# Performance work log

Measured on AMD Instinct MI355X. Metric: run time of the kernel, lower is better.

## Reference

```python
import jax, jax.numpy as jnp
import numpy as np

N_NODES = 100000
N_EDGES = 600000
D = 128
BN_EPS = 1e-5


def setup_inputs() -> dict:
    key = jax.random.key(0)
    k1, k2, k3 = jax.random.split(key, 3)
    x = jax.random.normal(k1, (N_NODES, D), dtype=jnp.float32)
    edge_index = jax.random.randint(k2, (2, N_EDGES), 0, N_NODES, dtype=jnp.int64)
    # Linear(in=D, out=D): kaiming-uniform-ish init
    W = jax.random.normal(k3, (D, D), dtype=jnp.float32) / np.sqrt(D)
    b = jnp.zeros((D,), dtype=jnp.float32)
    eps_gin = jnp.zeros((), dtype=jnp.float32)  # train_eps=True, init 0
    gamma = jnp.ones((D,), dtype=jnp.float32)
    beta = jnp.zeros((D,), dtype=jnp.float32)
    return {"x": x, "edge_index": edge_index, "W": W, "b": b,
            "eps_gin": eps_gin, "gamma": gamma, "beta": beta}


def reference(x, edge_index, W, b, eps_gin, gamma, beta):
    src, dst = edge_index[0], edge_index[1]
    # GIN aggregation: sum of source features into destination nodes
    agg = jax.ops.segment_sum(x[src], dst, num_segments=N_NODES)  # [N, D]
    h = (1.0 + eps_gin) * x + agg
    # MLP([D, D]) == single Linear (PyG plain_last)
    h = jnp.einsum('nd,df->nf', h, W.T) + b  # torch Linear: h @ W^T + b
    # BatchNorm1d in training mode (batch stats, biased variance)
    mean = jnp.mean(h, axis=0)
    var = jnp.mean((h - mean) ** 2, axis=0)
    h = (h - mean) * jax.lax.rsqrt(var + BN_EPS) * gamma + beta
    h = jax.nn.relu(h)
    # residual
    return h + x
```

## Files before the change

kernel.cpp:

```cpp
#include <hip/hip_runtime.h>
#include <hip/hip_bf16.h>

#define N_NODES 100000
#define N_EDGES 600000
#define D 128
#define BN_EPS 1e-5f
#define CAP 32
#define NAGG_BLOCKS 1024

typedef __bf16 bf16x8 __attribute__((ext_vector_type(8)));
typedef float floatx4 __attribute__((ext_vector_type(4)));
typedef unsigned short ushortx8 __attribute__((ext_vector_type(8)));

__device__ __forceinline__ unsigned short f2bf(float f) {
    union { float f; unsigned u; } v; v.f = f;
    unsigned u = v.u;
    unsigned r = u + 0x7FFFu + ((u >> 16) & 1u);
    return (unsigned short)(r >> 16);
}
__device__ __forceinline__ float bflo(unsigned u) {
    union { unsigned u; float f; } v; v.u = u << 16; return v.f;
}
__device__ __forceinline__ float bfhi(unsigned u) {
    union { unsigned u; float f; } v; v.u = u & 0xFFFF0000u; return v.f;
}

__global__ __launch_bounds__(256) void k_fill(const int* __restrict__ ei,
                                              int* __restrict__ cursor,
                                              int* __restrict__ bucket) {
    int e = blockIdx.x * 256 + threadIdx.x;
    if (e >= N_EDGES) return;
    int src = ei[e];
    int dst = ei[N_EDGES + e];
    int pos = atomicAdd(&cursor[dst], 1);
    if (pos < CAP) bucket[dst * CAP + pos] = src;
}

__global__ __launch_bounds__(256) void k_gemm_y(const float* __restrict__ x,
                                                const float* __restrict__ W,
                                                unsigned short* __restrict__ y) {
    const int lane = threadIdx.x & 63;
    const int wid  = threadIdx.x >> 6;
    const int gw   = blockIdx.x * 4 + wid;
    const int fhalf = gw & 1;
    const int chunk = gw >> 1;
    const int n16  = lane & 15;
    const int quad = lane >> 4;
    const int fbase = fhalf * 64;

    bf16x8 B[4][4];
#pragma unroll
    for (int ft = 0; ft < 4; ++ft) {
#pragma unroll
        for (int ks = 0; ks < 4; ++ks) {
            const float* wp = W + (fbase + ft * 16 + n16) * D + ks * 32 + quad * 8;
            float4 wa = *(const float4*)wp;
            float4 wb = *(const float4*)(wp + 4);
            ushortx8 u;
            u[0] = f2bf(wa.x); u[1] = f2bf(wa.y); u[2] = f2bf(wa.z); u[3] = f2bf(wa.w);
            u[4] = f2bf(wb.x); u[5] = f2bf(wb.y); u[6] = f2bf(wb.z); u[7] = f2bf(wb.w);
            B[ft][ks] = __builtin_bit_cast(bf16x8, u);
        }
    }

    const int rbase = chunk * 16;
    floatx4 acc[4];
#pragma unroll
    for (int ft = 0; ft < 4; ++ft) acc[ft] = (floatx4){0.f, 0.f, 0.f, 0.f};

#pragma unroll
    for (int ks = 0; ks < 4; ++ks) {
        const float* xp = x + (size_t)(rbase + n16) * D + ks * 32 + quad * 8;
        float4 xa = *(const float4*)xp;
        float4 xb4 = *(const float4*)(xp + 4);
        ushortx8 u;
        u[0] = f2bf(xa.x); u[1] = f2bf(xa.y); u[2] = f2bf(xa.z); u[3] = f2bf(xa.w);
        u[4] = f2bf(xb4.x); u[5] = f2bf(xb4.y); u[6] = f2bf(xb4.z); u[7] = f2bf(xb4.w);
        bf16x8 a = __builtin_bit_cast(bf16x8, u);
#pragma unroll
        for (int ft = 0; ft < 4; ++ft)
            acc[ft] = __builtin_amdgcn_mfma_f32_16x16x32_bf16(a, B[ft][ks], acc[ft], 0, 0, 0);
    }

#pragma unroll
    for (int ft = 0; ft < 4; ++ft) {
        const int col = fbase + ft * 16 + n16;
#pragma unroll
        for (int i = 0; i < 4; ++i)
            y[(size_t)(rbase + quad * 4 + i) * D + col] = f2bf(acc[ft][i]);
    }
}

__global__ __launch_bounds__(256) void k_agg_y(const int* __restrict__ cursor,
                                               const int* __restrict__ bucket,
                                               const unsigned short* __restrict__ y,
                                               const float* __restrict__ epsp,
                                               unsigned short* __restrict__ zb,
                                               float* __restrict__ pscr) {
    const int t = threadIdx.x;
    const int lane = t & 31;
    const int slot = t >> 5;
    const float one_eps = 1.0f + epsp[0];

    float psum[4] = {0.f, 0.f, 0.f, 0.f};
    float psq[4]  = {0.f, 0.f, 0.f, 0.f};

    for (int base = blockIdx.x * 8; base < N_NODES; base += NAGG_BLOCKS * 8) {
        const int node = base + slot;
        int deg = cursor[node];
        if (deg > CAP) deg = CAP;
        const int* bk = bucket + node * CAP;

        float4 a0 = make_float4(0.f, 0.f, 0.f, 0.f);
        float4 a1 = a0, a2 = a0, a3 = a0, a4 = a0, a5 = a0, a6 = a0, a7 = a0;

        for (int i = 0; i < deg; i += 8) {
            int rem = deg - i, last = rem - 1;
            int s0 = bk[i];
            int s1 = bk[i + (1 < rem ? 1 : last)];
            int s2 = bk[i + (2 < rem ? 2 : last)];
            int s3 = bk[i + (3 < rem ? 3 : last)];
            int s4 = bk[i + (4 < rem ? 4 : last)];
            int s5 = bk[i + (5 < rem ? 5 : last)];
            int s6 = bk[i + (6 < rem ? 6 : last)];
            int s7 = bk[i + (7 < rem ? 7 : last)];
            uint2 v0 = ((const uint2*)(y + (size_t)s0 * D))[lane];
            uint2 v1 = ((const uint2*)(y + (size_t)s1 * D))[lane];
            uint2 v2 = ((const uint2*)(y + (size_t)s2 * D))[lane];
            uint2 v3 = ((const uint2*)(y + (size_t)s3 * D))[lane];
            uint2 v4 = ((const uint2*)(y + (size_t)s4 * D))[lane];
            uint2 v5 = ((const uint2*)(y + (size_t)s5 * D))[lane];
            uint2 v6 = ((const uint2*)(y + (size_t)s6 * D))[lane];
            uint2 v7 = ((const uint2*)(y + (size_t)s7 * D))[lane];
            a0.x += bflo(v0.x); a0.y += bfhi(v0.x); a0.z += bflo(v0.y); a0.w += bfhi(v0.y);
            if (1 < rem) { a1.x += bflo(v1.x); a1.y += bfhi(v1.x); a1.z += bflo(v1.y); a1.w += bfhi(v1.y); }
            if (2 < rem) { a2.x += bflo(v2.x); a2.y += bfhi(v2.x); a2.z += bflo(v2.y); a2.w += bfhi(v2.y); }
            if (3 < rem) { a3.x += bflo(v3.x); a3.y += bfhi(v3.x); a3.z += bflo(v3.y); a3.w += bfhi(v3.y); }
            if (4 < rem) { a4.x += bflo(v4.x); a4.y += bfhi(v4.x); a4.z += bflo(v4.y); a4.w += bfhi(v4.y); }
            if (5 < rem) { a5.x += bflo(v5.x); a5.y += bfhi(v5.x); a5.z += bflo(v5.y); a5.w += bfhi(v5.y); }
            if (6 < rem) { a6.x += bflo(v6.x); a6.y += bfhi(v6.x); a6.z += bflo(v6.y); a6.w += bfhi(v6.y); }
            if (7 < rem) { a7.x += bflo(v7.x); a7.y += bfhi(v7.x); a7.z += bflo(v7.y); a7.w += bfhi(v7.y); }
        }
        float r0 = ((a0.x + a1.x) + (a2.x + a3.x)) + ((a4.x + a5.x) + (a6.x + a7.x));
        float r1 = ((a0.y + a1.y) + (a2.y + a3.y)) + ((a4.y + a5.y) + (a6.y + a7.y));
        float r2 = ((a0.z + a1.z) + (a2.z + a3.z)) + ((a4.z + a5.z) + (a6.z + a7.z));
        float r3 = ((a0.w + a1.w) + (a2.w + a3.w)) + ((a4.w + a5.w) + (a6.w + a7.w));

        uint2 yv = ((const uint2*)(y + (size_t)node * D))[lane];
        float z0 = one_eps * bflo(yv.x) + r0;
        float z1 = one_eps * bfhi(yv.x) + r1;
        float z2 = one_eps * bflo(yv.y) + r2;
        float z3 = one_eps * bfhi(yv.y) + r3;

        ushort4 o;
        o.x = f2bf(z0); o.y = f2bf(z1); o.z = f2bf(z2); o.w = f2bf(z3);
        ((ushort4*)(zb + (size_t)node * D))[lane] = o;

        psum[0] += z0; psq[0] += z0 * z0;
        psum[1] += z1; psq[1] += z1 * z1;
        psum[2] += z2; psq[2] += z2 * z2;
        psum[3] += z3; psq[3] += z3 * z3;
    }

    __shared__ float sred[8][32][8];
#pragma unroll
    for (int j = 0; j < 4; ++j) {
        sred[slot][lane][j]     = psum[j];
        sred[slot][lane][4 + j] = psq[j];
    }
    __syncthreads();
    {
        const int c = t & 127;
        const int j = (t < 128) ? (c & 3) : 4 + (c & 3);
        const int l = c >> 2;
        float acc = 0.f;
#pragma unroll
        for (int s = 0; s < 8; ++s)
            acc += sred[s][l][j];
        pscr[(size_t)blockIdx.x * 256 + t] = acc;
    }
}

__global__ __launch_bounds__(256) void k_bnreduce(const float* __restrict__ pscr,
                                                  float* __restrict__ part2) {
    const int t = threadIdx.x;
    const int b = blockIdx.x;
    float acc = 0.f;
    const float* p = pscr + (size_t)b * (NAGG_BLOCKS / 32) * 256 + t;
#pragma unroll 8
    for (int s = 0; s < NAGG_BLOCKS / 32; ++s)
        acc += p[(size_t)s * 256];
    part2[b * 256 + t] = acc;
}

__global__ __launch_bounds__(256) void k_final(const unsigned short* __restrict__ zb,
                                               const float* __restrict__ x,
                                               const float* __restrict__ part2,
                                               const float* __restrict__ gamma,
                                               const float* __restrict__ beta,
                                               float* __restrict__ out) {
    __shared__ float red[256];
    __shared__ float scs[128], shs[128];
    const int t = threadIdx.x;
    {
        float acc = 0.f;
#pragma unroll 8
        for (int j = 0; j < 32; ++j)
            acc += part2[j * 256 + t];
        red[t] = acc;
    }
    __syncthreads();
    if (t < 128) {
        const float inv_n = 1.0f / (float)N_NODES;
        float mean = red[t] * inv_n;
        float var  = red[128 + t] * inv_n - mean * mean;
        float s    = gamma[t] * rsqrtf(var + BN_EPS);
        scs[t] = s;
        shs[t] = beta[t] - mean * s;
    }
    __syncthreads();

    for (size_t i = (size_t)blockIdx.x * 256 + t; i < (size_t)N_NODES * D / 4;
         i += (size_t)gridDim.x * 256) {
        const size_t idx = i * 4;
        const int f = (int)(idx & (D - 1));
        uint2 zv = *(const uint2*)(zb + idx);
        float4 xv = *(const float4*)(x + idx);
        float z0 = bflo(zv.x), z1 = bfhi(zv.x), z2 = bflo(zv.y), z3 = bfhi(zv.y);
        float4 o;
        o.x = fmaxf(z0 * scs[f]     + shs[f],     0.f) + xv.x;
        o.y = fmaxf(z1 * scs[f + 1] + shs[f + 1], 0.f) + xv.y;
        o.z = fmaxf(z2 * scs[f + 2] + shs[f + 2], 0.f) + xv.z;
        o.w = fmaxf(z3 * scs[f + 3] + shs[f + 3], 0.f) + xv.w;
        *(float4*)(out + idx) = o;
    }
}

extern "C" void kernel_launch(void* const* d_in, const int* in_sizes, int n_in,
                              void* d_out, int out_size, void* d_ws, size_t ws_size,
                              hipStream_t stream) {
    const float* x     = (const float*)d_in[0];
    const int*   ei    = (const int*)d_in[1];
    const float* W     = (const float*)d_in[2];
    const float* epsp  = (const float*)d_in[4];
    const float* gamma = (const float*)d_in[5];
    const float* beta  = (const float*)d_in[6];
    float* out = (float*)d_out;

    char* ws = (char*)d_ws;
    int*   cursor = (int*)ws;
    int*   bucket = (int*)(ws + 400000ull);
    unsigned short* y  = (unsigned short*)(ws + 13200000ull);
    unsigned short* zb = (unsigned short*)(ws + 38800000ull);
    float* pscr  = (float*)(ws + 64400000ull);
    float* part2 = (float*)ws;

    hipMemsetAsync(cursor, 0, 400000ull, stream);

    k_fill<<<(N_EDGES + 255) / 256, 256, 0, stream>>>(ei, cursor, bucket);
    k_gemm_y<<<3125, 256, 0, stream>>>(x, W, y);
    k_agg_y<<<NAGG_BLOCKS, 256, 0, stream>>>(cursor, bucket, y, epsp, zb, pscr);
    k_bnreduce<<<32, 256, 0, stream>>>(pscr, part2);
    k_final<<<2048, 256, 0, stream>>>(zb, x, part2, gamma, beta, out);
}
```

Measured before the change: 261.3 us.

## Split aggregation from BN stats, batch edge fill, persist GEMM waves

```diff
diff --git a/kernel.cpp b/kernel.cpp
--- a/kernel.cpp
+++ b/kernel.cpp
@@ -6,7 +6,10 @@
 #define D 128
 #define BN_EPS 1e-5f
 #define CAP 32
-#define NAGG_BLOCKS 1024
+#define GEMM_BLOCKS 1024
+#define GEMM_NSLOTS (GEMM_BLOCKS * 2)
+#define FILL_THREADS 150000
+#define ZS_BLOCKS 256
 
 typedef __bf16 bf16x8 __attribute__((ext_vector_type(8)));
 typedef float floatx4 __attribute__((ext_vector_type(4)));
@@ -28,12 +31,21 @@
 __global__ __launch_bounds__(256) void k_fill(const int* __restrict__ ei,
                                               int* __restrict__ cursor,
                                               int* __restrict__ bucket) {
-    int e = blockIdx.x * 256 + threadIdx.x;
-    if (e >= N_EDGES) return;
-    int src = ei[e];
-    int dst = ei[N_EDGES + e];
-    int pos = atomicAdd(&cursor[dst], 1);
-    if (pos < CAP) bucket[dst * CAP + pos] = src;
+    int base = blockIdx.x * 256 + threadIdx.x;
+    if (base >= FILL_THREADS) return;
+    int e0 = base, e1 = base + FILL_THREADS, e2 = base + 2 * FILL_THREADS,
+        e3 = base + 3 * FILL_THREADS;
+    int s0 = ei[e0], s1 = ei[e1], s2 = ei[e2], s3 = ei[e3];
+    int d0 = ei[N_EDGES + e0], d1 = ei[N_EDGES + e1],
+        d2 = ei[N_EDGES + e2], d3 = ei[N_EDGES + e3];
+    int p0 = atomicAdd(&cursor[d0], 1);
+    int p1 = atomicAdd(&cursor[d1], 1);
+    int p2 = atomicAdd(&cursor[d2], 1);
+    int p3 = atomicAdd(&cursor[d3], 1);
+    if (p0 < CAP) bucket[d0 * CAP + p0] = s0;
+    if (p1 < CAP) bucket[d1 * CAP + p1] = s1;
+    if (p2 < CAP) bucket[d2 * CAP + p2] = s2;
+    if (p3 < CAP) bucket[d3 * CAP + p3] = s3;
 }
 
 __global__ __launch_bounds__(256) void k_gemm_y(const float* __restrict__ x,
@@ -43,7 +55,7 @@
     const int wid  = threadIdx.x >> 6;
     const int gw   = blockIdx.x * 4 + wid;
     const int fhalf = gw & 1;
-    const int chunk = gw >> 1;
+    const int pair  = gw >> 1;
     const int n16  = lane & 15;
     const int quad = lane >> 4;
     const int fbase = fhalf * 64;
@@ -63,106 +75,113 @@
         }
     }
 
-    const int rbase = chunk * 16;
-    floatx4 acc[4];
-#pragma unroll
-    for (int ft = 0; ft < 4; ++ft) acc[ft] = (floatx4){0.f, 0.f, 0.f, 0.f};
-
-#pragma unroll
-    for (int ks = 0; ks < 4; ++ks) {
-        const float* xp = x + (size_t)(rbase + n16) * D + ks * 32 + quad * 8;
-        float4 xa = *(const float4*)xp;
-        float4 xb4 = *(const float4*)(xp + 4);
-        ushortx8 u;
-        u[0] = f2bf(xa.x); u[1] = f2bf(xa.y); u[2] = f2bf(xa.z); u[3] = f2bf(xa.w);
-        u[4] = f2bf(xb4.x); u[5] = f2bf(xb4.y); u[6] = f2bf(xb4.z); u[7] = f2bf(xb4.w);
-        bf16x8 a = __builtin_bit_cast(bf16x8, u);
-#pragma unroll
-        for (int ft = 0; ft < 4; ++ft)
-            acc[ft] = __builtin_amdgcn_mfma_f32_16x16x32_bf16(a, B[ft][ks], acc[ft], 0, 0, 0);
-    }
-
-#pragma unroll
-    for (int ft = 0; ft < 4; ++ft) {
-        const int col = fbase + ft * 16 + n16;
-#pragma unroll
-        for (int i = 0; i < 4; ++i)
-            y[(size_t)(rbase + quad * 4 + i) * D + col] = f2bf(acc[ft][i]);
-    }
-}
-
-__global__ __launch_bounds__(256) void k_agg_y(const int* __restrict__ cursor,
-                                               const int* __restrict__ bucket,
-                                               const unsigned short* __restrict__ y,
-                                               const float* __restrict__ epsp,
-                                               unsigned short* __restrict__ zb,
-                                               float* __restrict__ pscr) {
+    for (int chunk = pair; chunk < N_NODES / 16; chunk += GEMM_NSLOTS) {
+        const int rbase = chunk * 16;
+        floatx4 acc[4];
+#pragma unroll
+        for (int ft = 0; ft < 4; ++ft) acc[ft] = (floatx4){0.f, 0.f, 0.f, 0.f};
+
+#pragma unroll
+        for (int ks = 0; ks < 4; ++ks) {
+            const float* xp = x + (size_t)(rbase + n16) * D + ks * 32 + quad * 8;
+            float4 xa = *(const float4*)xp;
+            float4 xb4 = *(const float4*)(xp + 4);
+            ushortx8 u;
+            u[0] = f2bf(xa.x); u[1] = f2bf(xa.y); u[2] = f2bf(xa.z); u[3] = f2bf(xa.w);
+            u[4] = f2bf(xb4.x); u[5] = f2bf(xb4.y); u[6] = f2bf(xb4.z); u[7] = f2bf(xb4.w);
+            bf16x8 a = __builtin_bit_cast(bf16x8, u);
+#pragma unroll
+            for (int ft = 0; ft < 4; ++ft)
+                acc[ft] = __builtin_amdgcn_mfma_f32_16x16x32_bf16(a, B[ft][ks], acc[ft], 0, 0, 0);
+        }
+
+#pragma unroll
+        for (int ft = 0; ft < 4; ++ft) {
+            const int col = fbase + ft * 16 + n16;
+#pragma unroll
+            for (int i = 0; i < 4; ++i)
+                y[(size_t)(rbase + quad * 4 + i) * D + col] = f2bf(acc[ft][i]);
+        }
+    }
+}
+
+__global__ __launch_bounds__(256) void k_agg(const int* __restrict__ cursor,
+                                             const int* __restrict__ bucket,
+                                             const unsigned short* __restrict__ y,
+                                             const float* __restrict__ epsp,
+                                             unsigned short* __restrict__ zb) {
+    int tid = blockIdx.x * 256 + threadIdx.x;
+    int node = tid >> 5;
+    if (node >= N_NODES) return;
+    int lane = tid & 31;
+    int deg = cursor[node];
+    if (deg > CAP) deg = CAP;
+    const int* bk = bucket + node * CAP;
+
+    float4 a0 = make_float4(0.f, 0.f, 0.f, 0.f);
+    float4 a1 = a0, a2 = a0, a3 = a0, a4 = a0, a5 = a0, a6 = a0, a7 = a0;
+
+    for (int i = 0; i < deg; i += 8) {
+        int rem = deg - i, last = rem - 1;
+        int s0 = bk[i];
+        int s1 = bk[i + (1 < rem ? 1 : last)];
+        int s2 = bk[i + (2 < rem ? 2 : last)];
+        int s3 = bk[i + (3 < rem ? 3 : last)];
+        int s4 = bk[i + (4 < rem ? 4 : last)];
+        int s5 = bk[i + (5 < rem ? 5 : last)];
+        int s6 = bk[i + (6 < rem ? 6 : last)];
+        int s7 = bk[i + (7 < rem ? 7 : last)];
+        uint2 v0 = ((const uint2*)(y + (size_t)s0 * D))[lane];
+        uint2 v1 = ((const uint2*)(y + (size_t)s1 * D))[lane];
+        uint2 v2 = ((const uint2*)(y + (size_t)s2 * D))[lane];
+        uint2 v3 = ((const uint2*)(y + (size_t)s3 * D))[lane];
+        uint2 v4 = ((const uint2*)(y + (size_t)s4 * D))[lane];
+        uint2 v5 = ((const uint2*)(y + (size_t)s5 * D))[lane];
+        uint2 v6 = ((const uint2*)(y + (size_t)s6 * D))[lane];
+        uint2 v7 = ((const uint2*)(y + (size_t)s7 * D))[lane];
+        a0.x += bflo(v0.x); a0.y += bfhi(v0.x); a0.z += bflo(v0.y); a0.w += bfhi(v0.y);
+        if (1 < rem) { a1.x += bflo(v1.x); a1.y += bfhi(v1.x); a1.z += bflo(v1.y); a1.w += bfhi(v1.y); }
+        if (2 < rem) { a2.x += bflo(v2.x); a2.y += bfhi(v2.x); a2.z += bflo(v2.y); a2.w += bfhi(v2.y); }
+        if (3 < rem) { a3.x += bflo(v3.x); a3.y += bfhi(v3.x); a3.z += bflo(v3.y); a3.w += bfhi(v3.y); }
+        if (4 < rem) { a4.x += bflo(v4.x); a4.y += bfhi(v4.x); a4.z += bflo(v4.y); a4.w += bfhi(v4.y); }
+        if (5 < rem) { a5.x += bflo(v5.x); a5.y += bfhi(v5.x); a5.z += bflo(v5.y); a5.w += bfhi(v5.y); }
+        if (6 < rem) { a6.x += bflo(v6.x); a6.y += bfhi(v6.x); a6.z += bflo(v6.y); a6.w += bfhi(v6.y); }
+        if (7 < rem) { a7.x += bflo(v7.x); a7.y += bfhi(v7.x); a7.z += bflo(v7.y); a7.w += bfhi(v7.y); }
+    }
+    float r0 = ((a0.x + a1.x) + (a2.x + a3.x)) + ((a4.x + a5.x) + (a6.x + a7.x));
+    float r1 = ((a0.y + a1.y) + (a2.y + a3.y)) + ((a4.y + a5.y) + (a6.y + a7.y));
+    float r2 = ((a0.z + a1.z) + (a2.z + a3.z)) + ((a4.z + a5.z) + (a6.z + a7.z));
+    float r3 = ((a0.w + a1.w) + (a2.w + a3.w)) + ((a4.w + a5.w) + (a6.w + a7.w));
+
+    const float one_eps = 1.0f + epsp[0];
+    uint2 yv = ((const uint2*)(y + (size_t)node * D))[lane];
+    ushort4 o;
+    o.x = f2bf(one_eps * bflo(yv.x) + r0);
+    o.y = f2bf(one_eps * bfhi(yv.x) + r1);
+    o.z = f2bf(one_eps * bflo(yv.y) + r2);
+    o.w = f2bf(one_eps * bfhi(yv.y) + r3);
+    ((ushort4*)(zb + (size_t)node * D))[lane] = o;
+}
+
+__global__ __launch_bounds__(256) void k_zstats(const unsigned short* __restrict__ zb,
+                                                float* __restrict__ pscr) {
     const int t = threadIdx.x;
     const int lane = t & 31;
     const int slot = t >> 5;
-    const float one_eps = 1.0f + epsp[0];
 
     float psum[4] = {0.f, 0.f, 0.f, 0.f};
     float psq[4]  = {0.f, 0.f, 0.f, 0.f};
 
-    for (int base = blockIdx.x * 8; base < N_NODES; base += NAGG_BLOCKS * 8) {
-        const int node = base + slot;
-        int deg = cursor[node];
-        if (deg > CAP) deg = CAP;
-        const int* bk = bucket + node * CAP;
-
-        float4 a0 = make_float4(0.f, 0.f, 0.f, 0.f);
-        float4 a1 = a0, a2 = a0, a3 = a0, a4 = a0, a5 = a0, a6 = a0, a7 = a0;
-
-        for (int i = 0; i < deg; i += 8) {
-            int rem = deg - i, last = rem - 1;
-            int s0 = bk[i];
-            int s1 = bk[i + (1 < rem ? 1 : last)];
-            int s2 = bk[i + (2 < rem ? 2 : last)];
-            int s3 = bk[i + (3 < rem ? 3 : last)];
-            int s4 = bk[i + (4 < rem ? 4 : last)];
-            int s5 = bk[i + (5 < rem ? 5 : last)];
-            int s6 = bk[i + (6 < rem ? 6 : last)];
-            int s7 = bk[i + (7 < rem ? 7 : last)];
-            uint2 v0 = ((const uint2*)(y + (size_t)s0 * D))[lane];
-            uint2 v1 = ((const uint2*)(y + (size_t)s1 * D))[lane];
-            uint2 v2 = ((const uint2*)(y + (size_t)s2 * D))[lane];
-            uint2 v3 = ((const uint2*)(y + (size_t)s3 * D))[lane];
-            uint2 v4 = ((const uint2*)(y + (size_t)s4 * D))[lane];
-            uint2 v5 = ((const uint2*)(y + (size_t)s5 * D))[lane];
-            uint2 v6 = ((const uint2*)(y + (size_t)s6 * D))[lane];
-            uint2 v7 = ((const uint2*)(y + (size_t)s7 * D))[lane];
-            a0.x += bflo(v0.x); a0.y += bfhi(v0.x); a0.z += bflo(v0.y); a0.w += bfhi(v0.y);
-            if (1 < rem) { a1.x += bflo(v1.x); a1.y += bfhi(v1.x); a1.z += bflo(v1.y); a1.w += bfhi(v1.y); }
-            if (2 < rem) { a2.x += bflo(v2.x); a2.y += bfhi(v2.x); a2.z += bflo(v2.y); a2.w += bfhi(v2.y); }
-            if (3 < rem) { a3.x += bflo(v3.x); a3.y += bfhi(v3.x); a3.z += bflo(v3.y); a3.w += bfhi(v3.y); }
-            if (4 < rem) { a4.x += bflo(v4.x); a4.y += bfhi(v4.x); a4.z += bflo(v4.y); a4.w += bfhi(v4.y); }
-            if (5 < rem) { a5.x += bflo(v5.x); a5.y += bfhi(v5.x); a5.z += bflo(v5.y); a5.w += bfhi(v5.y); }
-            if (6 < rem) { a6.x += bflo(v6.x); a6.y += bfhi(v6.x); a6.z += bflo(v6.y); a6.w += bfhi(v6.y); }
-            if (7 < rem) { a7.x += bflo(v7.x); a7.y += bfhi(v7.x); a7.z += bflo(v7.y); a7.w += bfhi(v7.y); }
-        }
-        float r0 = ((a0.x + a1.x) + (a2.x + a3.x)) + ((a4.x + a5.x) + (a6.x + a7.x));
-        float r1 = ((a0.y + a1.y) + (a2.y + a3.y)) + ((a4.y + a5.y) + (a6.y + a7.y));
-        float r2 = ((a0.z + a1.z) + (a2.z + a3.z)) + ((a4.z + a5.z) + (a6.z + a7.z));
-        float r3 = ((a0.w + a1.w) + (a2.w + a3.w)) + ((a4.w + a5.w) + (a6.w + a7.w));
-
-        uint2 yv = ((const uint2*)(y + (size_t)node * D))[lane];
-        float z0 = one_eps * bflo(yv.x) + r0;
-        float z1 = one_eps * bfhi(yv.x) + r1;
-        float z2 = one_eps * bflo(yv.y) + r2;
-        float z3 = one_eps * bfhi(yv.y) + r3;
-
-        ushort4 o;
-        o.x = f2bf(z0); o.y = f2bf(z1); o.z = f2bf(z2); o.w = f2bf(z3);
-        ((ushort4*)(zb + (size_t)node * D))[lane] = o;
-
+    for (int node = blockIdx.x * 8 + slot; node < N_NODES; node += ZS_BLOCKS * 8) {
+        uint2 zv = ((const uint2*)(zb + (size_t)node * D))[lane];
+        float z0 = bflo(zv.x), z1 = bfhi(zv.x), z2 = bflo(zv.y), z3 = bfhi(zv.y);
         psum[0] += z0; psq[0] += z0 * z0;
         psum[1] += z1; psq[1] += z1 * z1;
         psum[2] += z2; psq[2] += z2 * z2;
         psum[3] += z3; psq[3] += z3 * z3;
     }
 
-    __shared__ float sred[8][32][8];
+    __shared__ float sred[8][32][9];
 #pragma unroll
     for (int j = 0; j < 4; ++j) {
         sred[slot][lane][j]     = psum[j];
@@ -181,43 +200,35 @@
     }
 }
 
-__global__ __launch_bounds__(256) void k_bnreduce(const float* __restrict__ pscr,
-                                                  float* __restrict__ part2) {
+__global__ __launch_bounds__(256) void k_scsh(const float* __restrict__ pscr,
+                                              const float* __restrict__ gamma,
+                                              const float* __restrict__ beta,
+                                              float* __restrict__ scsh) {
     const int t = threadIdx.x;
-    const int b = blockIdx.x;
     float acc = 0.f;
-    const float* p = pscr + (size_t)b * (NAGG_BLOCKS / 32) * 256 + t;
-#pragma unroll 8
-    for (int s = 0; s < NAGG_BLOCKS / 32; ++s)
-        acc += p[(size_t)s * 256];
-    part2[b * 256 + t] = acc;
-}
-
-__global__ __launch_bounds__(256) void k_final(const unsigned short* __restrict__ zb,
-                                               const float* __restrict__ x,
-                                               const float* __restrict__ part2,
-                                               const float* __restrict__ gamma,
-                                               const float* __restrict__ beta,
-                                               float* __restrict__ out) {
+    for (int r = 0; r < ZS_BLOCKS; ++r)
+        acc += pscr[(size_t)r * 256 + t];
     __shared__ float red[256];
-    __shared__ float scs[128], shs[128];
-    const int t = threadIdx.x;
-    {
-        float acc = 0.f;
-#pragma unroll 8
-        for (int j = 0; j < 32; ++j)
-            acc += part2[j * 256 + t];
-        red[t] = acc;
-    }
+    red[t] = acc;
     __syncthreads();
     if (t < 128) {
         const float inv_n = 1.0f / (float)N_NODES;
         float mean = red[t] * inv_n;
         float var  = red[128 + t] * inv_n - mean * mean;
         float s    = gamma[t] * rsqrtf(var + BN_EPS);
-        scs[t] = s;
-        shs[t] = beta[t] - mean * s;
-    }
+        scsh[t]       = s;
+        scsh[128 + t] = beta[t] - mean * s;
+    }
+}
+
+__global__ __launch_bounds__(256) void k_final(const unsigned short* __restrict__ zb,
+                                               const float* __restrict__ x,
+                                               const float* __restrict__ scsh,
+                                               float* __restrict__ out) {
+    __shared__ float scs[128], shs[128];
+    const int t = threadIdx.x;
+    if (t < 128) scs[t] = scsh[t];
+    else         shs[t - 128] = scsh[t];
     __syncthreads();
 
     for (size_t i = (size_t)blockIdx.x * 256 + t; i < (size_t)N_NODES * D / 4;
@@ -249,17 +260,18 @@
 
     char* ws = (char*)d_ws;
     int*   cursor = (int*)ws;
-    int*   bucket = (int*)(ws + 400000ull);
-    unsigned short* y  = (unsigned short*)(ws + 13200000ull);
-    unsigned short* zb = (unsigned short*)(ws + 38800000ull);
-    float* pscr  = (float*)(ws + 64400000ull);
-    float* part2 = (float*)ws;
+    int*   bucket = (int*)(ws + 400128ull);
+    unsigned short* y  = (unsigned short*)(ws + 13200128ull);
+    unsigned short* zb = (unsigned short*)(ws + 38800128ull);
+    float* scsh = (float*)(ws + 64400128ull);
+    float* pscr = (float*)bucket;
 
     hipMemsetAsync(cursor, 0, 400000ull, stream);
 
-    k_fill<<<(N_EDGES + 255) / 256, 256, 0, stream>>>(ei, cursor, bucket);
-    k_gemm_y<<<3125, 256, 0, stream>>>(x, W, y);
-    k_agg_y<<<NAGG_BLOCKS, 256, 0, stream>>>(cursor, bucket, y, epsp, zb, pscr);
-    k_bnreduce<<<32, 256, 0, stream>>>(pscr, part2);
-    k_final<<<2048, 256, 0, stream>>>(zb, x, part2, gamma, beta, out);
-}
+    k_fill<<<(FILL_THREADS + 255) / 256, 256, 0, stream>>>(ei, cursor, bucket);
+    k_gemm_y<<<GEMM_BLOCKS, 256, 0, stream>>>(x, W, y);
+    k_agg<<<(N_NODES * 32 + 255) / 256, 256, 0, stream>>>(cursor, bucket, y, epsp, zb);
+    k_zstats<<<ZS_BLOCKS, 256, 0, stream>>>(zb, pscr);
+    k_scsh<<<1, 256, 0, stream>>>(pscr, gamma, beta, scsh);
+    k_final<<<2048, 256, 0, stream>>>(zb, x, scsh, out);
+}
```

Result: faster. 244.2 us (-6.6%).
